# Performance work log

Hardware: AMD Instinct MI355X
Metric: run time of the kernel (lower is better)

## Reference

```python
import jax, jax.numpy as jnp
import numpy as np


def setup_inputs() -> dict:
    key = jax.random.key(0)
    kx, ky, kw = jax.random.split(key, 3)
    B, N, M = 8, 4096, 4096
    x = jax.random.normal(kx, (B, N, 3), dtype=jnp.float32)
    y = jax.random.normal(ky, (B, M, 3), dtype=jnp.float32)
    weight = jax.random.uniform(kw, (B,), dtype=jnp.float32)
    return {"x": x, "y": y, "weight": weight}


def reference(x, y, weight):
    # (mathematically identical to sum((x-y)^2), avoids the (B,N,M,3) tensor)
    x2 = jnp.sum(x * x, axis=-1)                     # (B, N)
    y2 = jnp.sum(y * y, axis=-1)                     # (B, M)
    xy = jnp.einsum('bnd,bmd->bnm', x, y)            # (B, N, M)
    dist = jnp.maximum(x2[:, :, None] + y2[:, None, :] - 2.0 * xy, 0.0)
    dist_x_min = jnp.min(dist, axis=2)               # (B, N) nearest-in-y per x
    dist_y_min = jnp.min(dist, axis=1)               # (B, M) nearest-in-x per y
    # point_reduction='mean', bidirectional=True
    loss = jnp.mean(dist_x_min, axis=1) + jnp.mean(dist_y_min, axis=1)  # (B,)
    loss = loss * weight
    # batch_reduction='mean'
    return jnp.mean(loss)
```

## Files before the change

### kernel.cpp

```cpp
#include <hip/hip_runtime.h>
#include <math.h>


constexpr int BATCH = 8;
constexpr int NP    = 4096;
constexpr int T     = 512;
constexpr int QPB   = 256;
constexpr int KPT   = 8;
constexpr int S     = 16;
constexpr int TPS   = 256;

__global__ __launch_bounds__(T) void chamfer_main(
    const float* __restrict__ x, const float* __restrict__ y,
    const float* __restrict__ w, float* __restrict__ ps)
{
    const int bid = blockIdx.x;
    const int dir = bid >> 7;
    const int b   = (bid >> 4) & 7;
    const int qc  = bid & 15;

    const float* q = dir ? y : x;
    const float* t = dir ? x : y;

    __shared__ float4 ty[NP];
    __shared__ float  pmin[S][QPB];
    __shared__ float  qn[QPB];
    __shared__ float  rsum[8];

    const int tid = threadIdx.x;

    const float* tb = t + (size_t)b * NP * 3;
    for (int j = tid; j < NP; j += T) {
        float t0 = tb[3 * j + 0];
        float t1 = tb[3 * j + 1];
        float t2 = tb[3 * j + 2];
        ty[j] = make_float4(t0, t1, t2, fmaf(t0, t0, fmaf(t1, t1, t2 * t2)));
    }

    const int qrow  = tid & 31;
    const int slice = tid >> 5;
    const int n0 = b * NP + qc * QPB + qrow * KPT;
    const float4* qb = reinterpret_cast<const float4*>(q + (size_t)n0 * 3);
    float4 v0 = qb[0], v1 = qb[1], v2 = qb[2], v3 = qb[3], v4 = qb[4], v5 = qb[5];
    float px[KPT][3] = {
        {v0.x, v0.y, v0.z}, {v0.w, v1.x, v1.y},
        {v1.z, v1.w, v2.x}, {v2.y, v2.z, v2.w},
        {v3.x, v3.y, v3.z}, {v3.w, v4.x, v4.y},
        {v4.z, v4.w, v5.x}, {v5.y, v5.z, v5.w},
    };
    float xn[KPT][3], mn[KPT];
    #pragma unroll
    for (int k = 0; k < KPT; ++k) {
        float x2 = fmaf(px[k][0], px[k][0],
                   fmaf(px[k][1], px[k][1], px[k][2] * px[k][2]));
        if (slice == 0) qn[qrow * KPT + k] = x2;
        #pragma unroll
        for (int d = 0; d < 3; ++d) xn[k][d] = -2.0f * px[k][d];
        mn[k] = INFINITY;
    }

    __syncthreads();

    const int j0 = slice * TPS;
    #pragma unroll 4
    for (int j = j0; j < j0 + TPS; j += 2) {
        float4 ta = ty[j];
        float4 tc = ty[j + 1];
        #pragma unroll
        for (int k = 0; k < KPT; ++k) {
            float da = fmaf(xn[k][0], ta.x,
                       fmaf(xn[k][1], ta.y, fmaf(xn[k][2], ta.z, ta.w)));
            float db = fmaf(xn[k][0], tc.x,
                       fmaf(xn[k][1], tc.y, fmaf(xn[k][2], tc.z, tc.w)));
            mn[k] = fminf(mn[k], fminf(da, db));
        }
    }

    #pragma unroll
    for (int k = 0; k < KPT; ++k) pmin[slice][qrow * KPT + k] = mn[k];
    __syncthreads();

    float val = 0.0f;
    if (tid < QPB) {
        float m = pmin[0][tid];
        #pragma unroll
        for (int s = 1; s < S; ++s) m = fminf(m, pmin[s][tid]);
        val = fmaxf(qn[tid] + m, 0.0f);
    }

    for (int off = 32; off; off >>= 1) val += __shfl_down(val, off, 64);
    if ((tid & 63) == 0) rsum[tid >> 6] = val;
    __syncthreads();
    if (tid == 0) {
        float s = ((rsum[0] + rsum[1]) + (rsum[2] + rsum[3]))
                + ((rsum[4] + rsum[5]) + (rsum[6] + rsum[7]));
        ps[bid] = s * w[b] * (1.0f / ((float)NP * (float)BATCH));
    }
}

__global__ __launch_bounds__(256) void chamfer_final(
    const float* __restrict__ ps, float* __restrict__ out)
{
    const int tid = threadIdx.x;
    float v = ps[tid];
    for (int off = 32; off; off >>= 1) v += __shfl_down(v, off, 64);
    __shared__ float red[4];
    if ((tid & 63) == 0) red[tid >> 6] = v;
    __syncthreads();
    if (tid == 0) out[0] = (red[0] + red[1]) + (red[2] + red[3]);
}

extern "C" void kernel_launch(void* const* d_in, const int* in_sizes, int n_in,
                              void* d_out, int out_size, void* d_ws, size_t ws_size,
                              hipStream_t stream) {
    const float* x = (const float*)d_in[0];
    const float* y = (const float*)d_in[1];
    const float* w = (const float*)d_in[2];
    float* out = (float*)d_out;
    float* ps  = (float*)d_ws;

    chamfer_main<<<256, T, 0, stream>>>(x, y, w, ps);
    chamfer_final<<<1, 256, 0, stream>>>(ps, out);
}
```

Measured before the change: 28.10 us.

## Fuse final reduction via fixed-point atomic accumulator with last-block finalize

Removes the second reduction kernel. Each block now converts its partial sum to 2^-44 fixed point and atomically adds it to a 64-bit accumulator whose top byte counts arriving blocks, and the last block writes the output. The per-slice minima are also pre-combined across wave halves with a cross-lane xor shuffle, which halves the shared-memory partial-min buffer. The trade is one kernel launch swapped for a memset plus a global atomic, and the fixed-point quantization relies on partial sums being non-negative and small enough to fit in 56 bits.

```diff
diff --git a/kernel.cpp b/kernel.cpp
--- a/kernel.cpp
+++ b/kernel.cpp
@@ -9,10 +9,12 @@
 constexpr int KPT   = 8;
 constexpr int S     = 16;
 constexpr int TPS   = 256;
+constexpr int NBLK  = 256;
 
 __global__ __launch_bounds__(T) void chamfer_main(
     const float* __restrict__ x, const float* __restrict__ y,
-    const float* __restrict__ w, float* __restrict__ ps)
+    const float* __restrict__ w, unsigned long long* __restrict__ acc,
+    float* __restrict__ out)
 {
     const int bid = blockIdx.x;
     const int dir = bid >> 7;
@@ -23,7 +25,7 @@
     const float* t = dir ? x : y;
 
     __shared__ float4 ty[NP];
-    __shared__ float  pmin[S][QPB];
+    __shared__ float  pmin[S / 2][QPB];
     __shared__ float  qn[QPB];
     __shared__ float  rsum[8];
 
@@ -77,14 +79,20 @@
     }
 
     #pragma unroll
-    for (int k = 0; k < KPT; ++k) pmin[slice][qrow * KPT + k] = mn[k];
+    for (int k = 0; k < KPT; ++k)
+        mn[k] = fminf(mn[k], __shfl_xor(mn[k], 32, 64));
+    if ((slice & 1) == 0) {
+        #pragma unroll
+        for (int k = 0; k < KPT; ++k)
+            pmin[slice >> 1][qrow * KPT + k] = mn[k];
+    }
     __syncthreads();
 
     float val = 0.0f;
     if (tid < QPB) {
         float m = pmin[0][tid];
         #pragma unroll
-        for (int s = 1; s < S; ++s) m = fminf(m, pmin[s][tid]);
+        for (int s = 1; s < S / 2; ++s) m = fminf(m, pmin[s][tid]);
         val = fmaxf(qn[tid] + m, 0.0f);
     }
 
@@ -94,20 +102,17 @@
     if (tid == 0) {
         float s = ((rsum[0] + rsum[1]) + (rsum[2] + rsum[3]))
                 + ((rsum[4] + rsum[5]) + (rsum[6] + rsum[7]));
-        ps[bid] = s * w[b] * (1.0f / ((float)NP * (float)BATCH));
+        s *= w[b] * (1.0f / ((float)NP * (float)BATCH));
+        unsigned long long fx =
+            (unsigned long long)llrintf(s * 17592186044416.0f);
+        unsigned long long add = (1ULL << 56) | fx;
+        unsigned long long old = atomicAdd(acc, add);
+        if ((old >> 56) == (unsigned long long)(NBLK - 1)) {
+            unsigned long long total = old + add;
+            double sum = (double)(total & ((1ULL << 56) - 1));
+            out[0] = (float)(sum * (1.0 / 17592186044416.0));
+        }
     }
-}
-
-__global__ __launch_bounds__(256) void chamfer_final(
-    const float* __restrict__ ps, float* __restrict__ out)
-{
-    const int tid = threadIdx.x;
-    float v = ps[tid];
-    for (int off = 32; off; off >>= 1) v += __shfl_down(v, off, 64);
-    __shared__ float red[4];
-    if ((tid & 63) == 0) red[tid >> 6] = v;
-    __syncthreads();
-    if (tid == 0) out[0] = (red[0] + red[1]) + (red[2] + red[3]);
 }
 
 extern "C" void kernel_launch(void* const* d_in, const int* in_sizes, int n_in,
@@ -117,8 +122,8 @@
     const float* y = (const float*)d_in[1];
     const float* w = (const float*)d_in[2];
     float* out = (float*)d_out;
-    float* ps  = (float*)d_ws;
+    unsigned long long* acc = (unsigned long long*)d_ws;
 
-    chamfer_main<<<256, T, 0, stream>>>(x, y, w, ps);
-    chamfer_final<<<1, 256, 0, stream>>>(ps, out);
+    hipMemsetAsync(acc, 0, sizeof(unsigned long long), stream);
+    chamfer_main<<<NBLK, T, 0, stream>>>(x, y, w, acc, out);
 }
```

Result: slower. 34.40 us (+22.5%).
